# Optimization experiments

Hardware: AMD Instinct MI355X
Metric: run time of the kernel (lower is better)

## Reference

```python
import jax, jax.numpy as jnp
import numpy as np

NUM_BLOCKS = 8
D_MODEL = 256
FLAT_DIM = NUM_BLOCKS * NUM_BLOCKS + NUM_BLOCKS * 4  # 96


def setup_inputs() -> dict:
    key = jax.random.key(0)
    k1, k2, k3, k4, k5 = jax.random.split(key, 5)
    B, S, Blk = 8, 16384, NUM_BLOCKS
    bit_tensor = jax.random.randint(k1, (B, S, Blk, 8), 0, 2, dtype=jnp.int32)
    macro_stimulus = jax.random.uniform(k2, (B, S), dtype=jnp.float32)
    # torch.rand(...) * 0.1 equivalent (diag masking done in reference, as in torch)
    W_init = jax.random.uniform(k3, (B, S, Blk, Blk), dtype=jnp.float32) * 0.1
    lin_w = jax.random.normal(k4, (D_MODEL, FLAT_DIM), dtype=jnp.float32) / np.sqrt(FLAT_DIM)
    lin_b = jax.random.normal(k5, (D_MODEL,), dtype=jnp.float32) * 0.01
    return {
        "bit_tensor": bit_tensor,
        "macro_stimulus": macro_stimulus,
        "W_init": W_init,
        "lin_w": lin_w,
        "lin_b": lin_b,
        "internal_steps": 10,
    }


def _decode_bits_to_epgl(bit_tensor):
    # [B,S,Blk,8] int bits -> [B,S,Blk,4] floats in {0, 1/3, 2/3, 1}
    b = bit_tensor.astype(jnp.float32)
    return (b[..., 0::2] * 2.0 + b[..., 1::2]) / 3.0  # pairs (0,1),(2,3),(4,5),(6,7) -> E,P,G,L


def _safe_pdist(h):
    # pairwise L2 over last dim: h [B,S,Blk,4] -> [B,S,Blk,Blk]; sqrt-safe at 0 (diagonal)
    diff = h[..., :, None, :] - h[..., None, :, :]
    d2 = jnp.sum(diff * diff, axis=-1)
    return jnp.where(d2 > 0, jnp.sqrt(jnp.where(d2 > 0, d2, 1.0)), 0.0)


def _step(h, W, stim, eye):
    clamp = lambda x: jnp.clip(x, 0.0, 1.0)
    E, P, G, L = h[..., 0], h[..., 1], h[..., 2], h[..., 3]
    W_ns = W * (1.0 - eye)
    inflow = jnp.matmul(W_ns, h)                         # [B,S,Blk,4]
    total_w = jnp.sum(W_ns, axis=-1, keepdims=True) + 1e-8
    neigh = inflow / total_w
    En, Pn, Gn, Ln = neigh[..., 0], neigh[..., 1], neigh[..., 2], neigh[..., 3]
    E_new = clamp(E + 0.3 * stim - 0.4 * P - 0.2 * G)
    P_new = clamp(P + 0.5 * stim + 0.3 * (Pn - P) - 0.2 * E)
    G_new = clamp(G + 0.4 * E * (1.0 - P) + 0.2 * (Gn - G) - 0.3 * P)
    good_neighbor = 0.5 * En + 0.5 * Gn
    L_new = clamp(L + 0.4 * good_neighbor + 0.3 * (Ln - L) - 0.3 * P)
    h_new = jnp.stack([E_new, P_new, G_new, L_new], axis=-1)
    h_diff = _safe_pdist(h_new)                          # cdist(h_new, h_new, p=2)
    mutual_L = (L_new[..., :, None] + L_new[..., None, :]) * 0.5
    W_new = clamp(W + 0.1 * mutual_L * h_diff - 0.05 * W) * (1.0 - eye)
    return h_new, W_new


def _forward(bit_tensor, macro_stimulus, W_init, lin_w, lin_b, internal_steps):
    B, S, Blk, _ = bit_tensor.shape
    eye = jnp.eye(Blk, dtype=jnp.float32)
    h = _decode_bits_to_epgl(bit_tensor)                 # [B,S,Blk,4]
    W = W_init * (1.0 - eye)                             # [B,S,Blk,Blk]
    stim = jnp.broadcast_to(macro_stimulus[..., None], (B, S, Blk))

    def body(carry, _):
        h, W = carry
        h, W = _step(h, W, stim, eye)
        return (h, W), None

    (h, W), _ = jax.lax.scan(body, (h, W), None, length=internal_steps)
    phys = jnp.concatenate([h.reshape(B, S, -1), W.reshape(B, S, -1)], axis=-1)  # [B,S,96]
    macro_embedding = jnp.einsum('bsf,df->bsd', phys, lin_w) + lin_b
    return macro_embedding, h, W


def reference(bit_tensor, macro_stimulus, W_init, lin_w, lin_b, internal_steps):
    return _forward(bit_tensor, macro_stimulus, W_init, lin_w, lin_b, internal_steps)
```

## Files before the change

### kernel.cpp

```cpp
#include <hip/hip_runtime.h>

#define NB 8
#define DM 256
#define FD 96
#define SLD 104

using half8 = _Float16 __attribute__((ext_vector_type(8)));
using half4 = _Float16 __attribute__((ext_vector_type(4)));
using f32x4 = float __attribute__((ext_vector_type(4)));
using f2    = float __attribute__((ext_vector_type(2)));

__device__ __forceinline__ float clamp01(float x) { return fminf(fmaxf(x, 0.0f), 1.0f); }

__device__ __forceinline__ float dpp_swap1(float x) {
    return __builtin_bit_cast(float,
        __builtin_amdgcn_mov_dpp(__builtin_bit_cast(int, x), 0xB1, 0xF, 0xF, true));
}

__global__ void bprep_kernel(const float* __restrict__ lin_w,
                             _Float16* __restrict__ Bpre)
{
    const int fb = blockIdx.x * 256 + threadIdx.x;
    const int ks = fb >> 10, nbv = (fb >> 6) & 15, ll = fb & 63;
    const float* lwrow = lin_w + (size_t)(nbv * 16 + (ll & 15)) * FD
                               + (ks * 32 + 4 * (ll >> 4));
    float4 lo = *reinterpret_cast<const float4*>(lwrow);
    float4 hi = *reinterpret_cast<const float4*>(lwrow + 16);
    half8 v;
    v[0] = (_Float16)lo.x; v[1] = (_Float16)lo.y; v[2] = (_Float16)lo.z; v[3] = (_Float16)lo.w;
    v[4] = (_Float16)hi.x; v[5] = (_Float16)hi.y; v[6] = (_Float16)hi.z; v[7] = (_Float16)hi.w;
    *reinterpret_cast<half8*>(Bpre + (size_t)fb * 8) = v;
}

__global__ __launch_bounds__(256, 2) void fused_kernel(
    const int* __restrict__ bits,
    const float* __restrict__ stim_in,
    const float* __restrict__ Winit,
    const int* __restrict__ steps_ptr,
    const _Float16* __restrict__ Bpre,
    const float* __restrict__ lin_b,
    float* __restrict__ out_emb,
    float* __restrict__ out_h,
    float* __restrict__ out_W)
{
    __shared__ __align__(16) char smem[64 * 132 * 4];
    _Float16* S    = reinterpret_cast<_Float16*>(smem);
    float*    Cbuf = reinterpret_cast<float*>(smem);

    const int tid  = threadIdx.x;
    const int pos0 = blockIdx.x * 128;
    const int p    = tid >> 1;
    const int pos  = pos0 + p;
    const int sub  = tid & 1;
    const int steps = steps_ptr[0];

    f2 hA[8];
    f2 hB[8];
    f2 W2[4][4];

    const int4* bp = reinterpret_cast<const int4*>(bits + (size_t)pos * 64 + sub * 32);
    #pragma unroll
    for (int b = 0; b < 4; ++b) {
        int4 lo = bp[2 * b + 0];
        int4 hi = bp[2 * b + 1];
        hA[b].x = (float)(lo.x * 2 + lo.y) / 3.0f;
        hA[b].y = (float)(lo.z * 2 + lo.w) / 3.0f;
        hB[b].x = (float)(hi.x * 2 + hi.y) / 3.0f;
        hB[b].y = (float)(hi.z * 2 + hi.w) / 3.0f;
    }
    #pragma unroll
    for (int b = 0; b < 4; ++b) {
        hA[4 + b].x = dpp_swap1(hA[b].x);
        hA[4 + b].y = dpp_swap1(hA[b].y);
        hB[4 + b].x = dpp_swap1(hB[b].x);
        hB[4 + b].y = dpp_swap1(hB[b].y);
    }

    const int co_own = sub * 4;
    const int co_oth = 4 - sub * 4;
    #pragma unroll
    for (int i = 0; i < 4; ++i) {
        const float* rowp = Winit + (size_t)pos * 64 + (size_t)(co_own + i) * 8;
        float4 a = *reinterpret_cast<const float4*>(rowp + co_own);
        float4 b = *reinterpret_cast<const float4*>(rowp + co_oth);
        W2[i][0] = (f2){a.x, a.y};
        W2[i][1] = (f2){a.z, a.w};
        W2[i][2] = (f2){b.x, b.y};
        W2[i][3] = (f2){b.z, b.w};
        if (i & 1) W2[i][i >> 1].y = 0.0f; else W2[i][i >> 1].x = 0.0f;
    }

    const float stim = stim_in[pos];

    constexpr int LEXT[4][4] = {{9,0,1,2},{9,9,3,4},{9,9,9,5},{9,9,9,9}};

    for (int st = 0; st < steps; ++st) {
        f2 nbA[4], nbB[4];
        #pragma unroll
        for (int i = 0; i < 4; ++i) {
            f2 sA = {0.f, 0.f}, sB = {0.f, 0.f};
            #pragma unroll
            for (int jc = 0; jc < 4; ++jc) {
                f2 wv = W2[i][jc];
                f2 w0 = {wv.x, wv.x};
                f2 w1 = {wv.y, wv.y};
                sA = __builtin_elementwise_fma(w0, hA[2 * jc],     sA);
                sA = __builtin_elementwise_fma(w1, hA[2 * jc + 1], sA);
                sB = __builtin_elementwise_fma(w0, hB[2 * jc],     sB);
                sB = __builtin_elementwise_fma(w1, hB[2 * jc + 1], sB);
            }
            float tw = W2[i][0].x; tw += W2[i][0].y;
            tw += W2[i][1].x;      tw += W2[i][1].y;
            tw += W2[i][2].x;      tw += W2[i][2].y;
            tw += W2[i][3].x;      tw += W2[i][3].y;
            float inv = __builtin_amdgcn_rcpf(tw + 1e-8f);
            f2 inv2 = {inv, inv};
            nbA[i] = sA * inv2;
            nbB[i] = sB * inv2;
        }
        #pragma unroll
        for (int i = 0; i < 4; ++i) {
            float E = hA[i].x, P = hA[i].y, G = hB[i].x, L = hB[i].y;
            float En = nbA[i].x, Pn = nbA[i].y, Gn = nbB[i].x, Ln = nbB[i].y;
            float E_new = clamp01(E + 0.3f * stim - 0.4f * P - 0.2f * G);
            float P_new = clamp01(P + 0.5f * stim + 0.3f * (Pn - P) - 0.2f * E);
            float G_new = clamp01(G + 0.4f * E * (1.0f - P) + 0.2f * (Gn - G) - 0.3f * P);
            float good  = 0.5f * En + 0.5f * Gn;
            float L_new = clamp01(L + 0.4f * good + 0.3f * (Ln - L) - 0.3f * P);
            hA[i] = (f2){E_new, P_new};
            hB[i] = (f2){G_new, L_new};
        }
        #pragma unroll
        for (int b = 0; b < 4; ++b) {
            hA[4 + b].x = dpp_swap1(hA[b].x);
            hA[4 + b].y = dpp_swap1(hA[b].y);
            hB[4 + b].x = dpp_swap1(hB[b].x);
            hB[4 + b].y = dpp_swap1(hB[b].y);
        }

        #pragma unroll
        for (int i = 0; i < 4; ++i) {
            #pragma unroll
            for (int j = i + 1; j < 4; ++j) {
                float d0 = hA[i].x - hA[j].x;
                float d1 = hA[i].y - hA[j].y;
                float d2 = hB[i].x - hB[j].x;
                float d3 = hB[i].y - hB[j].y;
                float q = d0 * d0 + d1 * d1 + d2 * d2 + d3 * d3;
                float dist = __builtin_amdgcn_sqrtf(q);
                float inc = 0.1f * (0.5f * (hB[i].y + hB[j].y)) * dist;
                float wij = (j & 1) ? W2[i][j >> 1].y : W2[i][j >> 1].x;
                wij = clamp01(wij + inc - 0.05f * wij);
                if (j & 1) W2[i][j >> 1].y = wij; else W2[i][j >> 1].x = wij;
                float wji = (i & 1) ? W2[j][i >> 1].y : W2[j][i >> 1].x;
                wji = clamp01(wji + inc - 0.05f * wji);
                if (i & 1) W2[j][i >> 1].y = wji; else W2[j][i >> 1].x = wji;
            }
        }
        #pragma unroll
        for (int u = 0; u < 4; ++u) {
            const int j = u + 4;
            float d0 = hA[u].x - hA[j].x;
            float d1 = hA[u].y - hA[j].y;
            float d2 = hB[u].x - hB[j].x;
            float d3 = hB[u].y - hB[j].y;
            float q = d0 * d0 + d1 * d1 + d2 * d2 + d3 * d3;
            float dist = __builtin_amdgcn_sqrtf(q);
            float inc = 0.1f * (0.5f * (hB[u].y + hB[j].y)) * dist;
            float wij = (j & 1) ? W2[u][j >> 1].y : W2[u][j >> 1].x;
            wij = clamp01(wij + inc - 0.05f * wij);
            if (j & 1) W2[u][j >> 1].y = wij; else W2[u][j >> 1].x = wij;
        }
        float cinc[6];
        #pragma unroll
        for (int u = 0; u < 4; ++u) {
            #pragma unroll
            for (int v = u + 1; v < 4; ++v) {
                const int k = LEXT[u][v];
                const int j = v + 4;
                float d0 = hA[u].x - hA[j].x;
                float d1 = hA[u].y - hA[j].y;
                float d2 = hB[u].x - hB[j].x;
                float d3 = hB[u].y - hB[j].y;
                float q = d0 * d0 + d1 * d1 + d2 * d2 + d3 * d3;
                float dist = __builtin_amdgcn_sqrtf(q);
                float inc = 0.1f * (0.5f * (hB[u].y + hB[j].y)) * dist;
                cinc[k] = inc;
                float wij = (j & 1) ? W2[u][j >> 1].y : W2[u][j >> 1].x;
                wij = clamp01(wij + inc - 0.05f * wij);
                if (j & 1) W2[u][j >> 1].y = wij; else W2[u][j >> 1].x = wij;
            }
        }
        float rinc[6];
        #pragma unroll
        for (int k = 0; k < 6; ++k) rinc[k] = dpp_swap1(cinc[k]);
        #pragma unroll
        for (int u = 0; u < 4; ++u) {
            #pragma unroll
            for (int v = 0; v < u; ++v) {
                const int k = LEXT[v][u];
                const int j = v + 4;
                float inc = rinc[k];
                float wij = (j & 1) ? W2[u][j >> 1].y : W2[u][j >> 1].x;
                wij = clamp01(wij + inc - 0.05f * wij);
                if (j & 1) W2[u][j >> 1].y = wij; else W2[u][j >> 1].x = wij;
            }
        }
    }

    {
        _Float16* sp = S + p * SLD;
        half8 v0, v1;
        v0[0] = (_Float16)hA[0].x; v0[1] = (_Float16)hA[0].y;
        v0[2] = (_Float16)hB[0].x; v0[3] = (_Float16)hB[0].y;
        v0[4] = (_Float16)hA[1].x; v0[5] = (_Float16)hA[1].y;
        v0[6] = (_Float16)hB[1].x; v0[7] = (_Float16)hB[1].y;
        v1[0] = (_Float16)hA[2].x; v1[1] = (_Float16)hA[2].y;
        v1[2] = (_Float16)hB[2].x; v1[3] = (_Float16)hB[2].y;
        v1[4] = (_Float16)hA[3].x; v1[5] = (_Float16)hA[3].y;
        v1[6] = (_Float16)hB[3].x; v1[7] = (_Float16)hB[3].y;
        *reinterpret_cast<half8*>(sp + sub * 16)     = v0;
        *reinterpret_cast<half8*>(sp + sub * 16 + 8) = v1;
        #pragma unroll
        for (int i = 0; i < 4; ++i) {
            half8 wv;
            #pragma unroll
            for (int gc = 0; gc < 8; ++gc) {
                const int lc0 = gc;
                const int lc1 = (gc + 4) & 7;
                float vs0 = (lc0 & 1) ? W2[i][lc0 >> 1].y : W2[i][lc0 >> 1].x;
                float vs1 = (lc1 & 1) ? W2[i][lc1 >> 1].y : W2[i][lc1 >> 1].x;
                wv[gc] = (_Float16)((sub == 0) ? vs0 : vs1);
            }
            *reinterpret_cast<half8*>(sp + 32 + (co_own + i) * 8) = wv;
        }
    }
    __syncthreads();

    #pragma unroll
    for (int i = 0; i < 4; ++i) {
        const int flat4 = i * 1024 + tid * 4;
        const int row = flat4 >> 5, feat = flat4 & 31;
        half4 v = *reinterpret_cast<const half4*>(S + row * SLD + feat);
        float4 o = make_float4((float)v[0], (float)v[1], (float)v[2], (float)v[3]);
        *reinterpret_cast<float4*>(out_h + (size_t)pos0 * 32 + flat4) = o;
    }
    #pragma unroll
    for (int i = 0; i < 8; ++i) {
        const int flat4 = i * 1024 + tid * 4;
        const int row = flat4 >> 6, feat = flat4 & 63;
        half4 v = *reinterpret_cast<const half4*>(S + row * SLD + 32 + feat);
        float4 o = make_float4((float)v[0], (float)v[1], (float)v[2], (float)v[3]);
        *reinterpret_cast<float4*>(out_W + (size_t)pos0 * 64 + flat4) = o;
    }

    const int w = tid >> 6, l = tid & 63;
    const int k0q = 4 * (l >> 4);
    half8 afr[2][3];
    #pragma unroll
    for (int t = 0; t < 2; ++t) {
        const int r = t * 64 + w * 16 + (l & 15);
        #pragma unroll
        for (int ks = 0; ks < 3; ++ks) {
            half4 lo = *reinterpret_cast<const half4*>(S + r * SLD + ks * 32 + k0q);
            half4 hi = *reinterpret_cast<const half4*>(S + r * SLD + ks * 32 + 16 + k0q);
            afr[t][ks] = __builtin_shufflevector(lo, hi, 0, 1, 2, 3, 4, 5, 6, 7);
        }
    }
    __syncthreads();

    #pragma unroll
    for (int t = 0; t < 2; ++t) {
        f32x4 acc[16];
        #pragma unroll
        for (int nbv = 0; nbv < 16; ++nbv) acc[nbv] = (f32x4){0.f, 0.f, 0.f, 0.f};
        #pragma unroll
        for (int ks = 0; ks < 3; ++ks) {
            #pragma unroll
            for (int nbv = 0; nbv < 16; ++nbv) {
                half8 b = *reinterpret_cast<const half8*>(Bpre + (size_t)((ks * 16 + nbv) * 64 + l) * 8);
                acc[nbv] = __builtin_amdgcn_mfma_f32_16x16x32_f16(afr[t][ks], b, acc[nbv], 0, 0, 0);
            }
        }
        #pragma unroll
        for (int c = 0; c < 2; ++c) {
            #pragma unroll
            for (int nn = 0; nn < 8; ++nn) {
                const int nbv = c * 8 + nn;
                #pragma unroll
                for (int r = 0; r < 4; ++r) {
                    const int row = w * 16 + 4 * (l >> 4) + r;
                    Cbuf[row * 132 + nn * 16 + (l & 15)] = acc[nbv][r];
                }
            }
            __syncthreads();
            const float4 biasv = reinterpret_cast<const float4*>(lin_b)[c * 32 + (l & 31)];
            #pragma unroll
            for (int rep = 0; rep < 8; ++rep) {
                const int row = w * 16 + rep * 2 + (l >> 5);
                float4 v = *reinterpret_cast<const float4*>(Cbuf + row * 132 + (l & 31) * 4);
                v.x += biasv.x; v.y += biasv.y; v.z += biasv.z; v.w += biasv.w;
                *reinterpret_cast<float4*>(out_emb + (size_t)(pos0 + t * 64 + row) * DM
                                           + c * 128 + (l & 31) * 4) = v;
            }
            __syncthreads();
        }
    }
}

extern "C" void kernel_launch(void* const* d_in, const int* in_sizes, int n_in,
                              void* d_out, int out_size, void* d_ws, size_t ws_size,
                              hipStream_t stream) {
    const int*   bits  = (const int*)d_in[0];
    const float* stim  = (const float*)d_in[1];
    const float* Winit = (const float*)d_in[2];
    const float* lin_w = (const float*)d_in[3];
    const float* lin_b = (const float*)d_in[4];
    const int*   steps = (const int*)d_in[5];

    const int npos = in_sizes[1];

    float* out_emb = (float*)d_out;
    float* out_h   = out_emb + (size_t)npos * DM;
    float* out_W   = out_h + (size_t)npos * 32;
    _Float16* Bpre = (_Float16*)d_ws;

    hipLaunchKernelGGL(bprep_kernel, dim3(12), dim3(256), 0, stream, lin_w, Bpre);
    hipLaunchKernelGGL(fused_kernel, dim3(npos / 128), dim3(256), 0, stream,
                       bits, stim, Winit, steps, Bpre, lin_b,
                       out_emb, out_h, out_W);
}
```

Baseline: 71.42 us.

## Process two positions per thread and store MFMA results directly without LDS staging

```diff
diff --git a/kernel.cpp b/kernel.cpp
--- a/kernel.cpp
+++ b/kernel.cpp
@@ -43,182 +43,195 @@
     float* __restrict__ out_h,
     float* __restrict__ out_W)
 {
-    __shared__ __align__(16) char smem[64 * 132 * 4];
-    _Float16* S    = reinterpret_cast<_Float16*>(smem);
-    float*    Cbuf = reinterpret_cast<float*>(smem);
+    __shared__ __align__(16) _Float16 S[256 * SLD];
 
     const int tid  = threadIdx.x;
-    const int pos0 = blockIdx.x * 128;
+    const int pos0 = blockIdx.x * 256;
     const int p    = tid >> 1;
-    const int pos  = pos0 + p;
     const int sub  = tid & 1;
     const int steps = steps_ptr[0];
 
-    f2 hA[8];
-    f2 hB[8];
-    f2 W2[4][4];
-
-    const int4* bp = reinterpret_cast<const int4*>(bits + (size_t)pos * 64 + sub * 32);
-    #pragma unroll
-    for (int b = 0; b < 4; ++b) {
-        int4 lo = bp[2 * b + 0];
-        int4 hi = bp[2 * b + 1];
-        hA[b].x = (float)(lo.x * 2 + lo.y) / 3.0f;
-        hA[b].y = (float)(lo.z * 2 + lo.w) / 3.0f;
-        hB[b].x = (float)(hi.x * 2 + hi.y) / 3.0f;
-        hB[b].y = (float)(hi.z * 2 + hi.w) / 3.0f;
-    }
-    #pragma unroll
-    for (int b = 0; b < 4; ++b) {
-        hA[4 + b].x = dpp_swap1(hA[b].x);
-        hA[4 + b].y = dpp_swap1(hA[b].y);
-        hB[4 + b].x = dpp_swap1(hB[b].x);
-        hB[4 + b].y = dpp_swap1(hB[b].y);
-    }
+    f2 hA[2][8];
+    f2 hB[2][8];
+    f2 W2[2][4][4];
+    float stim[2];
 
     const int co_own = sub * 4;
     const int co_oth = 4 - sub * 4;
-    #pragma unroll
-    for (int i = 0; i < 4; ++i) {
-        const float* rowp = Winit + (size_t)pos * 64 + (size_t)(co_own + i) * 8;
-        float4 a = *reinterpret_cast<const float4*>(rowp + co_own);
-        float4 b = *reinterpret_cast<const float4*>(rowp + co_oth);
-        W2[i][0] = (f2){a.x, a.y};
-        W2[i][1] = (f2){a.z, a.w};
-        W2[i][2] = (f2){b.x, b.y};
-        W2[i][3] = (f2){b.z, b.w};
-        if (i & 1) W2[i][i >> 1].y = 0.0f; else W2[i][i >> 1].x = 0.0f;
-    }
-
-    const float stim = stim_in[pos];
+
+    #pragma unroll
+    for (int q = 0; q < 2; ++q) {
+        const int pos = pos0 + q * 128 + p;
+        const int4* bp = reinterpret_cast<const int4*>(bits + (size_t)pos * 64 + sub * 32);
+        #pragma unroll
+        for (int b = 0; b < 4; ++b) {
+            int4 lo = bp[2 * b + 0];
+            int4 hi = bp[2 * b + 1];
+            hA[q][b].x = (float)(lo.x * 2 + lo.y) / 3.0f;
+            hA[q][b].y = (float)(lo.z * 2 + lo.w) / 3.0f;
+            hB[q][b].x = (float)(hi.x * 2 + hi.y) / 3.0f;
+            hB[q][b].y = (float)(hi.z * 2 + hi.w) / 3.0f;
+        }
+        #pragma unroll
+        for (int b = 0; b < 4; ++b) {
+            hA[q][4 + b].x = dpp_swap1(hA[q][b].x);
+            hA[q][4 + b].y = dpp_swap1(hA[q][b].y);
+            hB[q][4 + b].x = dpp_swap1(hB[q][b].x);
+            hB[q][4 + b].y = dpp_swap1(hB[q][b].y);
+        }
+        #pragma unroll
+        for (int i = 0; i < 4; ++i) {
+            const float* rowp = Winit + (size_t)pos * 64 + (size_t)(co_own + i) * 8;
+            float4 a = *reinterpret_cast<const float4*>(rowp + co_own);
+            float4 b = *reinterpret_cast<const float4*>(rowp + co_oth);
+            W2[q][i][0] = (f2){a.x, a.y};
+            W2[q][i][1] = (f2){a.z, a.w};
+            W2[q][i][2] = (f2){b.x, b.y};
+            W2[q][i][3] = (f2){b.z, b.w};
+            if (i & 1) W2[q][i][i >> 1].y = 0.0f; else W2[q][i][i >> 1].x = 0.0f;
+        }
+        stim[q] = stim_in[pos];
+    }
 
     constexpr int LEXT[4][4] = {{9,0,1,2},{9,9,3,4},{9,9,9,5},{9,9,9,9}};
 
     for (int st = 0; st < steps; ++st) {
-        f2 nbA[4], nbB[4];
-        #pragma unroll
-        for (int i = 0; i < 4; ++i) {
-            f2 sA = {0.f, 0.f}, sB = {0.f, 0.f};
-            #pragma unroll
-            for (int jc = 0; jc < 4; ++jc) {
-                f2 wv = W2[i][jc];
-                f2 w0 = {wv.x, wv.x};
-                f2 w1 = {wv.y, wv.y};
-                sA = __builtin_elementwise_fma(w0, hA[2 * jc],     sA);
-                sA = __builtin_elementwise_fma(w1, hA[2 * jc + 1], sA);
-                sB = __builtin_elementwise_fma(w0, hB[2 * jc],     sB);
-                sB = __builtin_elementwise_fma(w1, hB[2 * jc + 1], sB);
-            }
-            float tw = W2[i][0].x; tw += W2[i][0].y;
-            tw += W2[i][1].x;      tw += W2[i][1].y;
-            tw += W2[i][2].x;      tw += W2[i][2].y;
-            tw += W2[i][3].x;      tw += W2[i][3].y;
-            float inv = __builtin_amdgcn_rcpf(tw + 1e-8f);
-            f2 inv2 = {inv, inv};
-            nbA[i] = sA * inv2;
-            nbB[i] = sB * inv2;
-        }
-        #pragma unroll
-        for (int i = 0; i < 4; ++i) {
-            float E = hA[i].x, P = hA[i].y, G = hB[i].x, L = hB[i].y;
-            float En = nbA[i].x, Pn = nbA[i].y, Gn = nbB[i].x, Ln = nbB[i].y;
-            float E_new = clamp01(E + 0.3f * stim - 0.4f * P - 0.2f * G);
-            float P_new = clamp01(P + 0.5f * stim + 0.3f * (Pn - P) - 0.2f * E);
-            float G_new = clamp01(G + 0.4f * E * (1.0f - P) + 0.2f * (Gn - G) - 0.3f * P);
-            float good  = 0.5f * En + 0.5f * Gn;
-            float L_new = clamp01(L + 0.4f * good + 0.3f * (Ln - L) - 0.3f * P);
-            hA[i] = (f2){E_new, P_new};
-            hB[i] = (f2){G_new, L_new};
-        }
-        #pragma unroll
-        for (int b = 0; b < 4; ++b) {
-            hA[4 + b].x = dpp_swap1(hA[b].x);
-            hA[4 + b].y = dpp_swap1(hA[b].y);
-            hB[4 + b].x = dpp_swap1(hB[b].x);
-            hB[4 + b].y = dpp_swap1(hB[b].y);
-        }
-
-        #pragma unroll
-        for (int i = 0; i < 4; ++i) {
-            #pragma unroll
-            for (int j = i + 1; j < 4; ++j) {
-                float d0 = hA[i].x - hA[j].x;
-                float d1 = hA[i].y - hA[j].y;
-                float d2 = hB[i].x - hB[j].x;
-                float d3 = hB[i].y - hB[j].y;
-                float q = d0 * d0 + d1 * d1 + d2 * d2 + d3 * d3;
-                float dist = __builtin_amdgcn_sqrtf(q);
-                float inc = 0.1f * (0.5f * (hB[i].y + hB[j].y)) * dist;
-                float wij = (j & 1) ? W2[i][j >> 1].y : W2[i][j >> 1].x;
+        f2 nbA[2][4], nbB[2][4];
+        #pragma unroll
+        for (int q = 0; q < 2; ++q) {
+            #pragma unroll
+            for (int i = 0; i < 4; ++i) {
+                f2 sA = {0.f, 0.f}, sB = {0.f, 0.f};
+                #pragma unroll
+                for (int jc = 0; jc < 4; ++jc) {
+                    f2 wv = W2[q][i][jc];
+                    f2 w0 = {wv.x, wv.x};
+                    f2 w1 = {wv.y, wv.y};
+                    sA = __builtin_elementwise_fma(w0, hA[q][2 * jc],     sA);
+                    sA = __builtin_elementwise_fma(w1, hA[q][2 * jc + 1], sA);
+                    sB = __builtin_elementwise_fma(w0, hB[q][2 * jc],     sB);
+                    sB = __builtin_elementwise_fma(w1, hB[q][2 * jc + 1], sB);
+                }
+                float tw = W2[q][i][0].x; tw += W2[q][i][0].y;
+                tw += W2[q][i][1].x;      tw += W2[q][i][1].y;
+                tw += W2[q][i][2].x;      tw += W2[q][i][2].y;
+                tw += W2[q][i][3].x;      tw += W2[q][i][3].y;
+                float inv = __builtin_amdgcn_rcpf(tw + 1e-8f);
+                f2 inv2 = {inv, inv};
+                nbA[q][i] = sA * inv2;
+                nbB[q][i] = sB * inv2;
+            }
+        }
+        #pragma unroll
+        for (int q = 0; q < 2; ++q) {
+            #pragma unroll
+            for (int i = 0; i < 4; ++i) {
+                float E = hA[q][i].x, P = hA[q][i].y, G = hB[q][i].x, L = hB[q][i].y;
+                float En = nbA[q][i].x, Pn = nbA[q][i].y, Gn = nbB[q][i].x, Ln = nbB[q][i].y;
+                float E_new = clamp01(E + 0.3f * stim[q] - 0.4f * P - 0.2f * G);
+                float P_new = clamp01(P + 0.5f * stim[q] + 0.3f * (Pn - P) - 0.2f * E);
+                float G_new = clamp01(G + 0.4f * E * (1.0f - P) + 0.2f * (Gn - G) - 0.3f * P);
+                float good  = 0.5f * En + 0.5f * Gn;
+                float L_new = clamp01(L + 0.4f * good + 0.3f * (Ln - L) - 0.3f * P);
+                hA[q][i] = (f2){E_new, P_new};
+                hB[q][i] = (f2){G_new, L_new};
+            }
+        }
+        #pragma unroll
+        for (int q = 0; q < 2; ++q) {
+            #pragma unroll
+            for (int b = 0; b < 4; ++b) {
+                hA[q][4 + b].x = dpp_swap1(hA[q][b].x);
+                hA[q][4 + b].y = dpp_swap1(hA[q][b].y);
+                hB[q][4 + b].x = dpp_swap1(hB[q][b].x);
+                hB[q][4 + b].y = dpp_swap1(hB[q][b].y);
+            }
+        }
+        #pragma unroll
+        for (int q = 0; q < 2; ++q) {
+            #pragma unroll
+            for (int i = 0; i < 4; ++i) {
+                #pragma unroll
+                for (int j = i + 1; j < 4; ++j) {
+                    float d0 = hA[q][i].x - hA[q][j].x;
+                    float d1 = hA[q][i].y - hA[q][j].y;
+                    float d2 = hB[q][i].x - hB[q][j].x;
+                    float d3 = hB[q][i].y - hB[q][j].y;
+                    float qd = d0 * d0 + d1 * d1 + d2 * d2 + d3 * d3;
+                    float dist = __builtin_amdgcn_sqrtf(qd);
+                    float inc = 0.1f * (0.5f * (hB[q][i].y + hB[q][j].y)) * dist;
+                    float wij = (j & 1) ? W2[q][i][j >> 1].y : W2[q][i][j >> 1].x;
+                    wij = clamp01(wij + inc - 0.05f * wij);
+                    if (j & 1) W2[q][i][j >> 1].y = wij; else W2[q][i][j >> 1].x = wij;
+                    float wji = (i & 1) ? W2[q][j][i >> 1].y : W2[q][j][i >> 1].x;
+                    wji = clamp01(wji + inc - 0.05f * wji);
+                    if (i & 1) W2[q][j][i >> 1].y = wji; else W2[q][j][i >> 1].x = wji;
+                }
+            }
+            #pragma unroll
+            for (int u = 0; u < 4; ++u) {
+                const int j = u + 4;
+                float d0 = hA[q][u].x - hA[q][j].x;
+                float d1 = hA[q][u].y - hA[q][j].y;
+                float d2 = hB[q][u].x - hB[q][j].x;
+                float d3 = hB[q][u].y - hB[q][j].y;
+                float qd = d0 * d0 + d1 * d1 + d2 * d2 + d3 * d3;
+                float dist = __builtin_amdgcn_sqrtf(qd);
+                float inc = 0.1f * (0.5f * (hB[q][u].y + hB[q][j].y)) * dist;
+                float wij = (j & 1) ? W2[q][u][j >> 1].y : W2[q][u][j >> 1].x;
                 wij = clamp01(wij + inc - 0.05f * wij);
-                if (j & 1) W2[i][j >> 1].y = wij; else W2[i][j >> 1].x = wij;
-                float wji = (i & 1) ? W2[j][i >> 1].y : W2[j][i >> 1].x;
-                wji = clamp01(wji + inc - 0.05f * wji);
-                if (i & 1) W2[j][i >> 1].y = wji; else W2[j][i >> 1].x = wji;
-            }
-        }
-        #pragma unroll
-        for (int u = 0; u < 4; ++u) {
-            const int j = u + 4;
-            float d0 = hA[u].x - hA[j].x;
-            float d1 = hA[u].y - hA[j].y;
-            float d2 = hB[u].x - hB[j].x;
-            float d3 = hB[u].y - hB[j].y;
-            float q = d0 * d0 + d1 * d1 + d2 * d2 + d3 * d3;
-            float dist = __builtin_amdgcn_sqrtf(q);
-            float inc = 0.1f * (0.5f * (hB[u].y + hB[j].y)) * dist;
-            float wij = (j & 1) ? W2[u][j >> 1].y : W2[u][j >> 1].x;
-            wij = clamp01(wij + inc - 0.05f * wij);
-            if (j & 1) W2[u][j >> 1].y = wij; else W2[u][j >> 1].x = wij;
-        }
-        float cinc[6];
-        #pragma unroll
-        for (int u = 0; u < 4; ++u) {
-            #pragma unroll
-            for (int v = u + 1; v < 4; ++v) {
-                const int k = LEXT[u][v];
-                const int j = v + 4;
-                float d0 = hA[u].x - hA[j].x;
-                float d1 = hA[u].y - hA[j].y;
-                float d2 = hB[u].x - hB[j].x;
-                float d3 = hB[u].y - hB[j].y;
-                float q = d0 * d0 + d1 * d1 + d2 * d2 + d3 * d3;
-                float dist = __builtin_amdgcn_sqrtf(q);
-                float inc = 0.1f * (0.5f * (hB[u].y + hB[j].y)) * dist;
-                cinc[k] = inc;
-                float wij = (j & 1) ? W2[u][j >> 1].y : W2[u][j >> 1].x;
-                wij = clamp01(wij + inc - 0.05f * wij);
-                if (j & 1) W2[u][j >> 1].y = wij; else W2[u][j >> 1].x = wij;
-            }
-        }
-        float rinc[6];
-        #pragma unroll
-        for (int k = 0; k < 6; ++k) rinc[k] = dpp_swap1(cinc[k]);
-        #pragma unroll
-        for (int u = 0; u < 4; ++u) {
-            #pragma unroll
-            for (int v = 0; v < u; ++v) {
-                const int k = LEXT[v][u];
-                const int j = v + 4;
-                float inc = rinc[k];
-                float wij = (j & 1) ? W2[u][j >> 1].y : W2[u][j >> 1].x;
-                wij = clamp01(wij + inc - 0.05f * wij);
-                if (j & 1) W2[u][j >> 1].y = wij; else W2[u][j >> 1].x = wij;
-            }
-        }
-    }
-
-    {
-        _Float16* sp = S + p * SLD;
+                if (j & 1) W2[q][u][j >> 1].y = wij; else W2[q][u][j >> 1].x = wij;
+            }
+            float cinc[6];
+            #pragma unroll
+            for (int u = 0; u < 4; ++u) {
+                #pragma unroll
+                for (int v = u + 1; v < 4; ++v) {
+                    const int k = LEXT[u][v];
+                    const int j = v + 4;
+                    float d0 = hA[q][u].x - hA[q][j].x;
+                    float d1 = hA[q][u].y - hA[q][j].y;
+                    float d2 = hB[q][u].x - hB[q][j].x;
+                    float d3 = hB[q][u].y - hB[q][j].y;
+                    float qd = d0 * d0 + d1 * d1 + d2 * d2 + d3 * d3;
+                    float dist = __builtin_amdgcn_sqrtf(qd);
+                    float inc = 0.1f * (0.5f * (hB[q][u].y + hB[q][j].y)) * dist;
+                    cinc[k] = inc;
+                    float wij = (j & 1) ? W2[q][u][j >> 1].y : W2[q][u][j >> 1].x;
+                    wij = clamp01(wij + inc - 0.05f * wij);
+                    if (j & 1) W2[q][u][j >> 1].y = wij; else W2[q][u][j >> 1].x = wij;
+                }
+            }
+            float rinc[6];
+            #pragma unroll
+            for (int k = 0; k < 6; ++k) rinc[k] = dpp_swap1(cinc[k]);
+            #pragma unroll
+            for (int u = 0; u < 4; ++u) {
+                #pragma unroll
+                for (int v = 0; v < u; ++v) {
+                    const int k = LEXT[v][u];
+                    const int j = v + 4;
+                    float inc = rinc[k];
+                    float wij = (j & 1) ? W2[q][u][j >> 1].y : W2[q][u][j >> 1].x;
+                    wij = clamp01(wij + inc - 0.05f * wij);
+                    if (j & 1) W2[q][u][j >> 1].y = wij; else W2[q][u][j >> 1].x = wij;
+                }
+            }
+        }
+    }
+
+    #pragma unroll
+    for (int q = 0; q < 2; ++q) {
+        _Float16* sp = S + (size_t)(q * 128 + p) * SLD;
         half8 v0, v1;
-        v0[0] = (_Float16)hA[0].x; v0[1] = (_Float16)hA[0].y;
-        v0[2] = (_Float16)hB[0].x; v0[3] = (_Float16)hB[0].y;
-        v0[4] = (_Float16)hA[1].x; v0[5] = (_Float16)hA[1].y;
-        v0[6] = (_Float16)hB[1].x; v0[7] = (_Float16)hB[1].y;
-        v1[0] = (_Float16)hA[2].x; v1[1] = (_Float16)hA[2].y;
-        v1[2] = (_Float16)hB[2].x; v1[3] = (_Float16)hB[2].y;
-        v1[4] = (_Float16)hA[3].x; v1[5] = (_Float16)hA[3].y;
-        v1[6] = (_Float16)hB[3].x; v1[7] = (_Float16)hB[3].y;
+        v0[0] = (_Float16)hA[q][0].x; v0[1] = (_Float16)hA[q][0].y;
+        v0[2] = (_Float16)hB[q][0].x; v0[3] = (_Float16)hB[q][0].y;
+        v0[4] = (_Float16)hA[q][1].x; v0[5] = (_Float16)hA[q][1].y;
+        v0[6] = (_Float16)hB[q][1].x; v0[7] = (_Float16)hB[q][1].y;
+        v1[0] = (_Float16)hA[q][2].x; v1[1] = (_Float16)hA[q][2].y;
+        v1[2] = (_Float16)hB[q][2].x; v1[3] = (_Float16)hB[q][2].y;
+        v1[4] = (_Float16)hA[q][3].x; v1[5] = (_Float16)hA[q][3].y;
+        v1[6] = (_Float16)hB[q][3].x; v1[7] = (_Float16)hB[q][3].y;
         *reinterpret_cast<half8*>(sp + sub * 16)     = v0;
         *reinterpret_cast<half8*>(sp + sub * 16 + 8) = v1;
         #pragma unroll
@@ -228,8 +241,8 @@
             for (int gc = 0; gc < 8; ++gc) {
                 const int lc0 = gc;
                 const int lc1 = (gc + 4) & 7;
-                float vs0 = (lc0 & 1) ? W2[i][lc0 >> 1].y : W2[i][lc0 >> 1].x;
-                float vs1 = (lc1 & 1) ? W2[i][lc1 >> 1].y : W2[i][lc1 >> 1].x;
+                float vs0 = (lc0 & 1) ? W2[q][i][lc0 >> 1].y : W2[q][i][lc0 >> 1].x;
+                float vs1 = (lc1 & 1) ? W2[q][i][lc1 >> 1].y : W2[q][i][lc1 >> 1].x;
                 wv[gc] = (_Float16)((sub == 0) ? vs0 : vs1);
             }
             *reinterpret_cast<half8*>(sp + 32 + (co_own + i) * 8) = wv;
@@ -238,7 +251,7 @@
     __syncthreads();
 
     #pragma unroll
-    for (int i = 0; i < 4; ++i) {
+    for (int i = 0; i < 8; ++i) {
         const int flat4 = i * 1024 + tid * 4;
         const int row = flat4 >> 5, feat = flat4 & 31;
         half4 v = *reinterpret_cast<const half4*>(S + row * SLD + feat);
@@ -246,7 +259,7 @@
         *reinterpret_cast<float4*>(out_h + (size_t)pos0 * 32 + flat4) = o;
     }
     #pragma unroll
-    for (int i = 0; i < 8; ++i) {
+    for (int i = 0; i < 16; ++i) {
         const int flat4 = i * 1024 + tid * 4;
         const int row = flat4 >> 6, feat = flat4 & 63;
         half4 v = *reinterpret_cast<const half4*>(S + row * SLD + 32 + feat);
@@ -256,21 +269,21 @@
 
     const int w = tid >> 6, l = tid & 63;
     const int k0q = 4 * (l >> 4);
-    half8 afr[2][3];
-    #pragma unroll
-    for (int t = 0; t < 2; ++t) {
+    float blin[16];
+    #pragma unroll
+    for (int nbv = 0; nbv < 16; ++nbv)
+        blin[nbv] = lin_b[nbv * 16 + (l & 15)];
+
+    #pragma unroll
+    for (int t = 0; t < 4; ++t) {
         const int r = t * 64 + w * 16 + (l & 15);
+        half8 afr[3];
         #pragma unroll
         for (int ks = 0; ks < 3; ++ks) {
             half4 lo = *reinterpret_cast<const half4*>(S + r * SLD + ks * 32 + k0q);
             half4 hi = *reinterpret_cast<const half4*>(S + r * SLD + ks * 32 + 16 + k0q);
-            afr[t][ks] = __builtin_shufflevector(lo, hi, 0, 1, 2, 3, 4, 5, 6, 7);
-        }
-    }
-    __syncthreads();
-
-    #pragma unroll
-    for (int t = 0; t < 2; ++t) {
+            afr[ks] = __builtin_shufflevector(lo, hi, 0, 1, 2, 3, 4, 5, 6, 7);
+        }
         f32x4 acc[16];
         #pragma unroll
         for (int nbv = 0; nbv < 16; ++nbv) acc[nbv] = (f32x4){0.f, 0.f, 0.f, 0.f};
@@ -279,31 +292,15 @@
             #pragma unroll
             for (int nbv = 0; nbv < 16; ++nbv) {
                 half8 b = *reinterpret_cast<const half8*>(Bpre + (size_t)((ks * 16 + nbv) * 64 + l) * 8);
-                acc[nbv] = __builtin_amdgcn_mfma_f32_16x16x32_f16(afr[t][ks], b, acc[nbv], 0, 0, 0);
-            }
-        }
-        #pragma unroll
-        for (int c = 0; c < 2; ++c) {
-            #pragma unroll
-            for (int nn = 0; nn < 8; ++nn) {
-                const int nbv = c * 8 + nn;
-                #pragma unroll
-                for (int r = 0; r < 4; ++r) {
-                    const int row = w * 16 + 4 * (l >> 4) + r;
-                    Cbuf[row * 132 + nn * 16 + (l & 15)] = acc[nbv][r];
-                }
-            }
-            __syncthreads();
-            const float4 biasv = reinterpret_cast<const float4*>(lin_b)[c * 32 + (l & 31)];
-            #pragma unroll
-            for (int rep = 0; rep < 8; ++rep) {
-                const int row = w * 16 + rep * 2 + (l >> 5);
-                float4 v = *reinterpret_cast<const float4*>(Cbuf + row * 132 + (l & 31) * 4);
-                v.x += biasv.x; v.y += biasv.y; v.z += biasv.z; v.w += biasv.w;
-                *reinterpret_cast<float4*>(out_emb + (size_t)(pos0 + t * 64 + row) * DM
-                                           + c * 128 + (l & 31) * 4) = v;
-            }
-            __syncthreads();
+                acc[nbv] = __builtin_amdgcn_mfma_f32_16x16x32_f16(afr[ks], b, acc[nbv], 0, 0, 0);
+            }
+        }
+        #pragma unroll
+        for (int reg = 0; reg < 4; ++reg) {
+            float* outp = out_emb + (size_t)(pos0 + t * 64 + w * 16 + 4 * (l >> 4) + reg) * DM + (l & 15);
+            #pragma unroll
+            for (int nbv = 0; nbv < 16; ++nbv)
+                outp[nbv * 16] = acc[nbv][reg] + blin[nbv];
         }
     }
 }
@@ -326,7 +323,7 @@
     _Float16* Bpre = (_Float16*)d_ws;
 
     hipLaunchKernelGGL(bprep_kernel, dim3(12), dim3(256), 0, stream, lin_w, Bpre);
-    hipLaunchKernelGGL(fused_kernel, dim3(npos / 128), dim3(256), 0, stream,
+    hipLaunchKernelGGL(fused_kernel, dim3(npos / 256), dim3(256), 0, stream,
                        bits, stim, Winit, steps, Bpre, lin_b,
                        out_emb, out_h, out_W);
 }
```

Result: slower. 84.18 us (+17.9%).
